# Kernel optimization log

Measured on AMD Instinct MI355X. Metric: run time of the kernel, lower is better.

Reference implementation:

```python
import jax, jax.numpy as jnp
import numpy as np

N_HEADS = 4
D_K = 64
SCALE = D_K ** -0.5


def setup_inputs() -> dict:
    key = jax.random.key(0)
    ks = jax.random.split(key, 5)
    B, C, H, W = 16, 256, 32, 32
    x = jax.random.normal(ks[0], (B, C, H, W), dtype=jnp.float32)
    # projection: Linear(C, 3*h*d_k); stored as [in, out] so y = x @ W + b
    w_proj = jax.random.normal(ks[1], (C, 3 * N_HEADS * D_K), dtype=jnp.float32) * (C ** -0.5)
    b_proj = jax.random.normal(ks[2], (3 * N_HEADS * D_K,), dtype=jnp.float32) * 0.02
    w_out = jax.random.normal(ks[3], (N_HEADS * D_K, C), dtype=jnp.float32) * ((N_HEADS * D_K) ** -0.5)
    b_out = jax.random.normal(ks[4], (C,), dtype=jnp.float32) * 0.02
    return {"x": x, "w_proj": w_proj, "b_proj": b_proj, "w_out": w_out, "b_out": b_out}


def reference(x, w_proj, b_proj, w_out, b_out):
    b, c, h, w = x.shape
    s = h * w
    # [b, c, h, w] -> [b, s, c]  (matches view + permute in torch)
    xf = jnp.transpose(x.reshape(b, c, s), (0, 2, 1))
    # QKV projection -> [b, s, heads, 3*d_k]
    qkv = (xf @ w_proj + b_proj).reshape(b, s, N_HEADS, 3 * D_K)
    q, k, v = jnp.split(qkv, 3, axis=-1)  # each [b, s, heads, d_k]
    # scores [b, i, j, heads]; softmax over j (axis=2), as in the original
    attn = jnp.einsum('bihd,bjhd->bijh', q, k) * SCALE
    attn = jax.nn.softmax(attn, axis=2)
    res = jnp.einsum('bijh,bjhd->bihd', attn, v).reshape(b, s, N_HEADS * D_K)
    res = res @ w_out + b_out + xf  # residual added to un-normalized xf (norm is unused in source)
    return jnp.transpose(res, (0, 2, 1)).reshape(b, c, h, w)
```

## Files before the change

### kernel.cpp

```cpp
#include <hip/hip_runtime.h>
#include <hip/hip_bf16.h>
#include <stdint.h>

typedef float f32x4 __attribute__((ext_vector_type(4)));
typedef float f32x16 __attribute__((ext_vector_type(16)));
typedef __bf16 bf16x8 __attribute__((ext_vector_type(8)));
typedef unsigned short u16x8 __attribute__((ext_vector_type(8)));
typedef int i32x4 __attribute__((ext_vector_type(4)));

#define MFMA16(a, b, c) __builtin_amdgcn_mfma_f32_16x16x32_bf16(a, b, c, 0, 0, 0)
#define MFMA32(a, b, c) __builtin_amdgcn_mfma_f32_32x32x16_bf16(a, b, c, 0, 0, 0)

#define QSCALE 0.18033688011112042f

static __device__ __forceinline__ unsigned short f2bf(float f) {
    uint32_t u = __builtin_bit_cast(uint32_t, f);
    u = u + 0x7FFFu + ((u >> 16) & 1u);
    return (unsigned short)(u >> 16);
}

static __device__ __forceinline__ bf16x8 ldb8(const unsigned short* p) {
    return __builtin_bit_cast(bf16x8, *reinterpret_cast<const u16x8*>(p));
}

static __device__ __forceinline__ void gload16(const void* g, void* l) {
    __builtin_amdgcn_global_load_lds(
        (const __attribute__((address_space(1))) void*)g,
        (__attribute__((address_space(3))) void*)l,
        16, 0, 0);
}

__global__ __launch_bounds__(256) void k_tall(const float* __restrict__ x,
                                              const float* __restrict__ wp,
                                              const float* __restrict__ wo,
                                              unsigned short* __restrict__ xT,
                                              unsigned short* __restrict__ wpT,
                                              unsigned short* __restrict__ woT) {
    int bid = blockIdx.x;
    const float* src; unsigned short* dst; int Cc, nCT; int lb;
    if (bid < 1024)      { src = x;  dst = xT;  Cc = 1024; nCT = 16; lb = bid; }
    else if (bid < 1072) { src = wp; dst = wpT; Cc = 768;  nCT = 12; lb = bid - 1024; }
    else                 { src = wo; dst = woT; Cc = 256;  nCT = 4;  lb = bid - 1072; }
    int R = 256, nRT = 4;
    int ct = lb % nCT;
    int rt = (lb / nCT) % nRT;
    int b  = lb / (nCT * nRT);
    int t = threadIdx.x;
    __shared__ __align__(16) unsigned short tile[64][72];
    int tr = t >> 2, tc = (t & 3) * 16;
    const float* sp = src + ((size_t)(b * R + rt * 64 + tr)) * Cc + ct * 64 + tc;
#pragma unroll
    for (int j = 0; j < 4; ++j) {
        float4 v = reinterpret_cast<const float4*>(sp)[j];
        ushort4 hv; hv.x = f2bf(v.x); hv.y = f2bf(v.y); hv.z = f2bf(v.z); hv.w = f2bf(v.w);
        *reinterpret_cast<ushort4*>(&tile[tr][tc + 4 * j]) = hv;
    }
    __syncthreads();
    int c = t >> 2, rs = (t & 3) * 16;
    u16x8 o0, o1;
#pragma unroll
    for (int z = 0; z < 8; ++z) o0[z] = tile[rs + z][c];
#pragma unroll
    for (int z = 0; z < 8; ++z) o1[z] = tile[rs + 8 + z][c];
    unsigned short* dp = dst + ((size_t)b * Cc + ct * 64 + c) * R + rt * 64 + rs;
    *reinterpret_cast<u16x8*>(dp) = o0;
    *reinterpret_cast<u16x8*>(dp + 8) = o1;
}

__global__ __launch_bounds__(256) void k_gemm_qkv(const unsigned short* __restrict__ xT,
                                                  const unsigned short* __restrict__ wT,
                                                  const float* __restrict__ bias,
                                                  unsigned short* __restrict__ qkv) {
    int bid = blockIdx.x;
    int mt = bid / 6, nt = bid - mt * 6;
    int tid = threadIdx.x;
    int w = tid >> 6, l = tid & 63;
    int l15 = l & 15, lg = l >> 4;
    int wm = (w >> 1) * 64, wn = (w & 1) * 64;

    __shared__ __align__(16) unsigned short Al[128 * 32];
    __shared__ __align__(16) unsigned short Bl[128 * 32];

    f32x4 acc[4][4] = {};

    const char* Agb = (const char*)xT + (size_t)mt * 128 * 512;
    const char* Bgb = (const char*)wT + (size_t)nt * 128 * 512;
    int r0 = w * 32;
    size_t lrow_off = (size_t)(r0 + (l >> 2)) * 512 + (l & 3) * 16;

    for (int kt = 0; kt < 256; kt += 32) {
        __syncthreads();
        const char* ag = Agb + lrow_off + kt * 2;
        const char* bg = Bgb + lrow_off + kt * 2;
        gload16(ag,             (char*)Al + r0 * 64);
        gload16(ag + 16 * 512,  (char*)Al + r0 * 64 + 1024);
        gload16(bg,             (char*)Bl + r0 * 64);
        gload16(bg + 16 * 512,  (char*)Bl + r0 * 64 + 1024);
        __syncthreads();
        bf16x8 af[4], bfr[4];
#pragma unroll
        for (int mi = 0; mi < 4; ++mi)
            af[mi] = ldb8(&Al[(wm + mi * 16 + l15) * 32 + lg * 8]);
#pragma unroll
        for (int ni = 0; ni < 4; ++ni)
            bfr[ni] = ldb8(&Bl[(wn + ni * 16 + l15) * 32 + lg * 8]);
#pragma unroll
        for (int mi = 0; mi < 4; ++mi)
#pragma unroll
            for (int ni = 0; ni < 4; ++ni)
                acc[mi][ni] = MFMA16(af[mi], bfr[ni], acc[mi][ni]);
    }

#pragma unroll
    for (int ni = 0; ni < 4; ++ni) {
        int n = nt * 128 + wn + ni * 16 + l15;
        float bz = bias[n];
        float qs = ((n % 192) < 64) ? QSCALE : 1.0f;
#pragma unroll
        for (int mi = 0; mi < 4; ++mi) {
            int mg = mt * 128 + wm + mi * 16 + lg * 4;
            unsigned short* qp = qkv + (size_t)mg * 768 + n;
#pragma unroll
            for (int r = 0; r < 4; ++r)
                qp[(size_t)r * 768] = f2bf((acc[mi][ni][r] + bz) * qs);
        }
    }
}

__global__ __launch_bounds__(256) void k_vt(const unsigned short* __restrict__ qkv,
                                            unsigned short* __restrict__ vT) {
    int bid = blockIdx.x;
    int jt = bid & 15;
    int bh = bid >> 4;
    int h = bh & 3;
    size_t bb = (size_t)(bh >> 2) * 1024;
    int t = threadIdx.x;
    __shared__ __align__(16) unsigned short tile[64][72];
    int jr = t >> 2, ds = (t & 3) * 16;
    const unsigned short* sp = qkv + (bb + jt * 64 + jr) * 768 + h * 192 + 128 + ds;
    *reinterpret_cast<u16x8*>(&tile[jr][ds])     = *reinterpret_cast<const u16x8*>(sp);
    *reinterpret_cast<u16x8*>(&tile[jr][ds + 8]) = *reinterpret_cast<const u16x8*>(sp + 8);
    __syncthreads();
    int d = t >> 2, js = (t & 3) * 16;
    u16x8 o0, o1;
#pragma unroll
    for (int z = 0; z < 8; ++z) o0[z] = tile[js + z][d];
#pragma unroll
    for (int z = 0; z < 8; ++z) o1[z] = tile[js + 8 + z][d];
    unsigned short* dp = vT + ((size_t)bh * 64 + d) * 1024 + jt * 64 + js;
    *reinterpret_cast<u16x8*>(dp) = o0;
    *reinterpret_cast<u16x8*>(dp + 8) = o1;
}

#define PACKJK(SV, R, OUT) do { \
    int pa_, pb_, pc_, pd_; \
    asm("v_cvt_pk_bf16_f32 %0, %1, %2" : "=v"(pa_) : "v"(SV[R + 0]), "v"(SV[R + 1])); \
    asm("v_cvt_pk_bf16_f32 %0, %1, %2" : "=v"(pb_) : "v"(SV[R + 2]), "v"(SV[R + 3])); \
    asm("v_cvt_pk_bf16_f32 %0, %1, %2" : "=v"(pc_) : "v"(SV[R + 4]), "v"(SV[R + 5])); \
    asm("v_cvt_pk_bf16_f32 %0, %1, %2" : "=v"(pd_) : "v"(SV[R + 6]), "v"(SV[R + 7])); \
    int pu_ = hi ? pa_ : pc_;  int psu_ = __shfl_xor(pu_, 32); \
    int pv_ = hi ? pb_ : pd_;  int psv_ = __shfl_xor(pv_, 32); \
    i32x4 pri_ = { hi ? psu_ : pa_, hi ? psv_ : pb_, hi ? pc_ : psu_, hi ? pd_ : psv_ }; \
    OUT = __builtin_bit_cast(bf16x8, pri_); \
} while (0)

__global__ __launch_bounds__(128) void k_attn(const unsigned short* __restrict__ qkv,
                                              const unsigned short* __restrict__ vT,
                                              unsigned short* __restrict__ ao) {
    int bid = blockIdx.x;
    int qt = bid & 15;
    int h  = (bid >> 4) & 3;
    int b  = bid >> 6;
    int tid = threadIdx.x;
    int w = tid >> 6;
    int l = tid & 63;
    int l31 = l & 31;
    int hi = l >> 5;
    int x7 = l & 7;

    __shared__ __align__(16) unsigned short Kl[64 * 64];
    __shared__ __align__(16) unsigned short Vl[64 * 64];

    const size_t bb = (size_t)b * 1024;
    const int bh = b * 4 + h;

    bf16x8 qf[4];
    int qg0 = qt * 64 + w * 32 + l31;
#pragma unroll
    for (int dk = 0; dk < 4; ++dk)
        qf[dk] = ldb8(qkv + (bb + qg0) * 768 + h * 192 + dk * 16 + hi * 8);

    int colB[4];
#pragma unroll
    for (int c = 0; c < 4; ++c) colB[c] = ((2 * c + hi) ^ x7) * 8;

    int srow = w * 32 + (l >> 3);
    int gsw  = (l & 7) ^ (srow & 7);
    const unsigned short* ksrc = qkv + (bb + srow) * 768 + h * 192 + 64 + gsw * 8;
    const unsigned short* vsrc = vT + ((size_t)bh * 64 + srow) * 1024 + gsw * 8;

    float mrow = -1e30f, lrow = 0.0f;
    f32x16 oacc0 = {}, oacc1 = {};

    for (int jt = 0; jt < 1024; jt += 64) {
        __syncthreads();
#pragma unroll
        for (int i = 0; i < 4; ++i) {
            gload16(ksrc + (size_t)i * 8 * 768, (char*)Kl + (w * 32 + i * 8) * 128);
            gload16(vsrc + (size_t)i * 8 * 1024, (char*)Vl + (w * 32 + i * 8) * 128);
        }
        __syncthreads();

        f32x16 st0 = {}, st1 = {};
#pragma unroll
        for (int dk = 0; dk < 4; ++dk) {
            bf16x8 k0 = ldb8(&Kl[(l31) * 64 + colB[dk]]);
            bf16x8 k1 = ldb8(&Kl[(32 + l31) * 64 + colB[dk]]);
            st0 = MFMA32(k0, qf[dk], st0);
            st1 = MFMA32(k1, qf[dk], st1);
        }

        float pm = st0[0];
#pragma unroll
        for (int r = 1; r < 16; ++r) pm = fmaxf(pm, st0[r]);
#pragma unroll
        for (int r = 0; r < 16; ++r) pm = fmaxf(pm, st1[r]);
        pm = fmaxf(pm, __shfl_xor(pm, 32));

        if (!__all(pm - mrow <= 8.0f)) {
            float mn = fmaxf(mrow, pm);
            float ef = __builtin_amdgcn_exp2f(mrow - mn);
            mrow = mn;
            lrow *= ef;
#pragma unroll
            for (int r = 0; r < 16; ++r) {
                int qr = (r & 3) + 8 * (r >> 2) + hi * 4;
                float efq = __shfl(ef, qr);
                oacc0[r] *= efq;
                oacc1[r] *= efq;
            }
        }

        float rs = 0.0f;
#pragma unroll
        for (int r = 0; r < 16; ++r) { st0[r] = __builtin_amdgcn_exp2f(st0[r] - mrow); rs += st0[r]; }
#pragma unroll
        for (int r = 0; r < 16; ++r) { st1[r] = __builtin_amdgcn_exp2f(st1[r] - mrow); rs += st1[r]; }
        rs += __shfl_xor(rs, 32);
        lrow += rs;

        bf16x8 pf0, pf1, pf2, pf3;
        PACKJK(st0, 0, pf0);
        PACKJK(st0, 8, pf1);
        PACKJK(st1, 0, pf2);
        PACKJK(st1, 8, pf3);

#pragma unroll
        for (int jk = 0; jk < 4; ++jk) {
            bf16x8 pfk = (jk == 0) ? pf0 : (jk == 1) ? pf1 : (jk == 2) ? pf2 : pf3;
            bf16x8 v0 = ldb8(&Vl[(l31) * 64 + colB[jk]]);
            bf16x8 v1 = ldb8(&Vl[(32 + l31) * 64 + colB[jk]]);
            oacc0 = MFMA32(pfk, v0, oacc0);
            oacc1 = MFMA32(pfk, v1, oacc1);
        }

        ksrc += (size_t)64 * 768;
        vsrc += 64;
    }

    float rcp = 1.0f / lrow;
#pragma unroll
    for (int r = 0; r < 16; ++r) {
        int qr = (r & 3) + 8 * (r >> 2) + hi * 4;
        float lq = __shfl(rcp, qr);
        int qg = qt * 64 + w * 32 + qr;
        size_t o = (bb + qg) * 256 + h * 64 + l31;
        ao[o]      = f2bf(oacc0[r] * lq);
        ao[o + 32] = f2bf(oacc1[r] * lq);
    }
}

__global__ __launch_bounds__(256) void k_gemm_out(const unsigned short* __restrict__ aoin,
                                                  const unsigned short* __restrict__ wT,
                                                  const float* __restrict__ bias,
                                                  const float* __restrict__ x,
                                                  float* __restrict__ out) {
    int bid = blockIdx.x;
    int mt = bid >> 2, nt = bid & 3;
    int tid = threadIdx.x;
    int w = tid >> 6, l = tid & 63;
    int l15 = l & 15, lg = l >> 4;
    int wm = (w >> 1) * 32, wn = (w & 1) * 32;

    __shared__ __align__(16) unsigned short Al[64 * 32];
    __shared__ __align__(16) unsigned short Bl[64 * 32];

    f32x4 acc[2][2] = {};

    const char* Agb = (const char*)aoin + (size_t)mt * 64 * 512;
    const char* Bgb = (const char*)wT + (size_t)nt * 64 * 512;
    int r0 = w * 16;
    size_t lrow_off = (size_t)(r0 + (l >> 2)) * 512 + (l & 3) * 16;

    for (int kt = 0; kt < 256; kt += 32) {
        __syncthreads();
        gload16(Agb + lrow_off + kt * 2, (char*)Al + r0 * 64);
        gload16(Bgb + lrow_off + kt * 2, (char*)Bl + r0 * 64);
        __syncthreads();
        bf16x8 af[2], bfr[2];
#pragma unroll
        for (int mi = 0; mi < 2; ++mi)
            af[mi] = ldb8(&Al[(wm + mi * 16 + l15) * 32 + lg * 8]);
#pragma unroll
        for (int ni = 0; ni < 2; ++ni)
            bfr[ni] = ldb8(&Bl[(wn + ni * 16 + l15) * 32 + lg * 8]);
#pragma unroll
        for (int mi = 0; mi < 2; ++mi)
#pragma unroll
            for (int ni = 0; ni < 2; ++ni)
                acc[mi][ni] = MFMA16(af[mi], bfr[ni], acc[mi][ni]);
    }

#pragma unroll
    for (int ni = 0; ni < 2; ++ni) {
        int n = nt * 64 + wn + ni * 16 + l15;
        float bz = bias[n];
#pragma unroll
        for (int mi = 0; mi < 2; ++mi) {
            int mg = mt * 64 + wm + mi * 16 + lg * 4;
            int bI = mg >> 10, i = mg & 1023;
            size_t o = (((size_t)(bI * 256 + n)) << 10) + i;
            float4 xr = *reinterpret_cast<const float4*>(x + o);
            float4 res;
            res.x = acc[mi][ni][0] + bz + xr.x;
            res.y = acc[mi][ni][1] + bz + xr.y;
            res.z = acc[mi][ni][2] + bz + xr.z;
            res.w = acc[mi][ni][3] + bz + xr.w;
            *reinterpret_cast<float4*>(out + o) = res;
        }
    }
}

extern "C" void kernel_launch(void* const* d_in, const int* in_sizes, int n_in,
                              void* d_out, int out_size, void* d_ws, size_t ws_size,
                              hipStream_t stream) {
    const float* x      = (const float*)d_in[0];
    const float* w_proj = (const float*)d_in[1];
    const float* b_proj = (const float*)d_in[2];
    const float* w_out  = (const float*)d_in[3];
    const float* b_out  = (const float*)d_in[4];
    float* out = (float*)d_out;

    char* ws = (char*)d_ws;
    unsigned short* xT     = (unsigned short*)(ws);
    unsigned short* wprojT = (unsigned short*)(ws + 8388608);
    unsigned short* woutT  = (unsigned short*)(ws + 8781824);
    unsigned short* qkv    = (unsigned short*)(ws + 8912896);
    unsigned short* ao     = (unsigned short*)(ws + 34078720);
    unsigned short* vT     = xT;

    k_tall<<<1088, 256, 0, stream>>>(x, w_proj, w_out, xT, wprojT, woutT);
    k_gemm_qkv<<<768, 256, 0, stream>>>(xT, wprojT, b_proj, qkv);
    k_vt<<<1024, 256, 0, stream>>>(qkv, vT);
    k_attn<<<1024, 128, 0, stream>>>(qkv, vT, ao);
    k_gemm_out<<<1024, 256, 0, stream>>>(ao, woutT, b_out, x, out);
}
```

Baseline: 146.8 us.

## Fuse V transpose into QKV GEMM epilogue and enlarge output GEMM tiles

The QKV projection epilogue now writes the V columns straight into a transposed per-head layout in a separate workspace buffer, which removes the standalone V-transpose kernel and its extra read and write pass over V. The output projection GEMM moves from 64x64 to 128x128 tiles with 4x4 MFMA fragments per wave, cutting the block count by four and improving operand reuse. Costs: V stores become 4-element strided writes rather than coalesced rows, and the bigger output tiles launch fewer blocks and raise register pressure.

```diff
diff --git a/kernel.cpp b/kernel.cpp
--- a/kernel.cpp
+++ b/kernel.cpp
@@ -70,7 +70,8 @@
 __global__ __launch_bounds__(256) void k_gemm_qkv(const unsigned short* __restrict__ xT,
                                                   const unsigned short* __restrict__ wT,
                                                   const float* __restrict__ bias,
-                                                  unsigned short* __restrict__ qkv) {
+                                                  unsigned short* __restrict__ qkv,
+                                                  unsigned short* __restrict__ vT) {
     int bid = blockIdx.x;
     int mt = bid / 6, nt = bid - mt * 6;
     int tid = threadIdx.x;
@@ -113,43 +114,36 @@
 
 #pragma unroll
     for (int ni = 0; ni < 4; ++ni) {
-        int n = nt * 128 + wn + ni * 16 + l15;
+        int n0 = nt * 128 + wn + ni * 16;
+        int n  = n0 + l15;
+        int c0 = n0 % 192;
         float bz = bias[n];
-        float qs = ((n % 192) < 64) ? QSCALE : 1.0f;
-#pragma unroll
-        for (int mi = 0; mi < 4; ++mi) {
-            int mg = mt * 128 + wm + mi * 16 + lg * 4;
-            unsigned short* qp = qkv + (size_t)mg * 768 + n;
-#pragma unroll
-            for (int r = 0; r < 4; ++r)
-                qp[(size_t)r * 768] = f2bf((acc[mi][ni][r] + bz) * qs);
-        }
-    }
-}
-
-__global__ __launch_bounds__(256) void k_vt(const unsigned short* __restrict__ qkv,
-                                            unsigned short* __restrict__ vT) {
-    int bid = blockIdx.x;
-    int jt = bid & 15;
-    int bh = bid >> 4;
-    int h = bh & 3;
-    size_t bb = (size_t)(bh >> 2) * 1024;
-    int t = threadIdx.x;
-    __shared__ __align__(16) unsigned short tile[64][72];
-    int jr = t >> 2, ds = (t & 3) * 16;
-    const unsigned short* sp = qkv + (bb + jt * 64 + jr) * 768 + h * 192 + 128 + ds;
-    *reinterpret_cast<u16x8*>(&tile[jr][ds])     = *reinterpret_cast<const u16x8*>(sp);
-    *reinterpret_cast<u16x8*>(&tile[jr][ds + 8]) = *reinterpret_cast<const u16x8*>(sp + 8);
-    __syncthreads();
-    int d = t >> 2, js = (t & 3) * 16;
-    u16x8 o0, o1;
-#pragma unroll
-    for (int z = 0; z < 8; ++z) o0[z] = tile[js + z][d];
-#pragma unroll
-    for (int z = 0; z < 8; ++z) o1[z] = tile[js + 8 + z][d];
-    unsigned short* dp = vT + ((size_t)bh * 64 + d) * 1024 + jt * 64 + js;
-    *reinterpret_cast<u16x8*>(dp) = o0;
-    *reinterpret_cast<u16x8*>(dp + 8) = o1;
+        if (c0 >= 128) {
+            int hq = n / 192;
+            int d  = (n % 192) - 128;
+#pragma unroll
+            for (int mi = 0; mi < 4; ++mi) {
+                int mg = mt * 128 + wm + mi * 16 + lg * 4;
+                int bI = mg >> 10, s = mg & 1023;
+                ushort4 hv;
+                hv.x = f2bf(acc[mi][ni][0] + bz);
+                hv.y = f2bf(acc[mi][ni][1] + bz);
+                hv.z = f2bf(acc[mi][ni][2] + bz);
+                hv.w = f2bf(acc[mi][ni][3] + bz);
+                *reinterpret_cast<ushort4*>(vT + ((size_t)(bI * 4 + hq) * 64 + d) * 1024 + s) = hv;
+            }
+        } else {
+            float qs = (c0 < 64) ? QSCALE : 1.0f;
+#pragma unroll
+            for (int mi = 0; mi < 4; ++mi) {
+                int mg = mt * 128 + wm + mi * 16 + lg * 4;
+                unsigned short* qp = qkv + (size_t)mg * 768 + n;
+#pragma unroll
+                for (int r = 0; r < 4; ++r)
+                    qp[(size_t)r * 768] = f2bf((acc[mi][ni][r] + bz) * qs);
+            }
+        }
+    }
 }
 
 #define PACKJK(SV, R, OUT) do { \
@@ -286,48 +280,52 @@
                                                   const float* __restrict__ x,
                                                   float* __restrict__ out) {
     int bid = blockIdx.x;
-    int mt = bid >> 2, nt = bid & 3;
+    int mt = bid >> 1, nt = bid & 1;
     int tid = threadIdx.x;
     int w = tid >> 6, l = tid & 63;
     int l15 = l & 15, lg = l >> 4;
-    int wm = (w >> 1) * 32, wn = (w & 1) * 32;
-
-    __shared__ __align__(16) unsigned short Al[64 * 32];
-    __shared__ __align__(16) unsigned short Bl[64 * 32];
-
-    f32x4 acc[2][2] = {};
-
-    const char* Agb = (const char*)aoin + (size_t)mt * 64 * 512;
-    const char* Bgb = (const char*)wT + (size_t)nt * 64 * 512;
-    int r0 = w * 16;
+    int wm = (w >> 1) * 64, wn = (w & 1) * 64;
+
+    __shared__ __align__(16) unsigned short Al[128 * 32];
+    __shared__ __align__(16) unsigned short Bl[128 * 32];
+
+    f32x4 acc[4][4] = {};
+
+    const char* Agb = (const char*)aoin + (size_t)mt * 128 * 512;
+    const char* Bgb = (const char*)wT + (size_t)nt * 128 * 512;
+    int r0 = w * 32;
     size_t lrow_off = (size_t)(r0 + (l >> 2)) * 512 + (l & 3) * 16;
 
     for (int kt = 0; kt < 256; kt += 32) {
         __syncthreads();
-        gload16(Agb + lrow_off + kt * 2, (char*)Al + r0 * 64);
-        gload16(Bgb + lrow_off + kt * 2, (char*)Bl + r0 * 64);
-        __syncthreads();
-        bf16x8 af[2], bfr[2];
-#pragma unroll
-        for (int mi = 0; mi < 2; ++mi)
+        const char* ag = Agb + lrow_off + kt * 2;
+        const char* bg = Bgb + lrow_off + kt * 2;
+        gload16(ag,             (char*)Al + r0 * 64);
+        gload16(ag + 16 * 512,  (char*)Al + r0 * 64 + 1024);
+        gload16(bg,             (char*)Bl + r0 * 64);
+        gload16(bg + 16 * 512,  (char*)Bl + r0 * 64 + 1024);
+        __syncthreads();
+        bf16x8 af[4], bfr[4];
+#pragma unroll
+        for (int mi = 0; mi < 4; ++mi)
             af[mi] = ldb8(&Al[(wm + mi * 16 + l15) * 32 + lg * 8]);
 #pragma unroll
-        for (int ni = 0; ni < 2; ++ni)
+        for (int ni = 0; ni < 4; ++ni)
             bfr[ni] = ldb8(&Bl[(wn + ni * 16 + l15) * 32 + lg * 8]);
 #pragma unroll
-        for (int mi = 0; mi < 2; ++mi)
-#pragma unroll
-            for (int ni = 0; ni < 2; ++ni)
+        for (int mi = 0; mi < 4; ++mi)
+#pragma unroll
+            for (int ni = 0; ni < 4; ++ni)
                 acc[mi][ni] = MFMA16(af[mi], bfr[ni], acc[mi][ni]);
     }
 
 #pragma unroll
-    for (int ni = 0; ni < 2; ++ni) {
-        int n = nt * 64 + wn + ni * 16 + l15;
+    for (int ni = 0; ni < 4; ++ni) {
+        int n = nt * 128 + wn + ni * 16 + l15;
         float bz = bias[n];
 #pragma unroll
-        for (int mi = 0; mi < 2; ++mi) {
-            int mg = mt * 64 + wm + mi * 16 + lg * 4;
+        for (int mi = 0; mi < 4; ++mi) {
+            int mg = mt * 128 + wm + mi * 16 + lg * 4;
             int bI = mg >> 10, i = mg & 1023;
             size_t o = (((size_t)(bI * 256 + n)) << 10) + i;
             float4 xr = *reinterpret_cast<const float4*>(x + o);
@@ -357,11 +355,10 @@
     unsigned short* woutT  = (unsigned short*)(ws + 8781824);
     unsigned short* qkv    = (unsigned short*)(ws + 8912896);
     unsigned short* ao     = (unsigned short*)(ws + 34078720);
-    unsigned short* vT     = xT;
+    unsigned short* vT     = (unsigned short*)(ws + 42467328);
 
     k_tall<<<1088, 256, 0, stream>>>(x, w_proj, w_out, xT, wprojT, woutT);
-    k_gemm_qkv<<<768, 256, 0, stream>>>(xT, wprojT, b_proj, qkv);
-    k_vt<<<1024, 256, 0, stream>>>(qkv, vT);
+    k_gemm_qkv<<<768, 256, 0, stream>>>(xT, wprojT, b_proj, qkv, vT);
     k_attn<<<1024, 128, 0, stream>>>(qkv, vT, ao);
-    k_gemm_out<<<1024, 256, 0, stream>>>(ao, woutT, b_out, x, out);
-}
+    k_gemm_out<<<256, 256, 0, stream>>>(ao, woutT, b_out, x, out);
+}
```

Result: faster. 137.2 us (-6.5%).
